# Kernel tuning notes

Hardware: AMD Instinct MI355X
Metric: run time of the kernel (lower is better)

Reference implementation:

```python
import jax, jax.numpy as jnp
import numpy as np

N_LAYERS = 12
N_CH = 256
N_IN = 4
KS = 3
SPECT_CH = 640


def conv1d(x, w, b, dilation):
    # x: [B, T, Cin], w: [K, Cin, Cout] (WIO), SAME padding, given dilation
    y = jax.lax.conv_general_dilated(
        x, w, window_strides=(1,), padding='SAME',
        rhs_dilation=(dilation,), dimension_numbers=('NWC', 'WIO', 'NWC'))
    return y + b


def setup_inputs() -> dict:
    key = jax.random.key(0)
    ks = jax.random.split(key, 16)
    s = 0.02
    inp = {}
    inp['audio'] = jax.random.normal(ks[0], (8, 4096, N_IN), dtype=jnp.float32)
    inp['spect'] = jax.random.normal(ks[1], (8, 4096, SPECT_CH), dtype=jnp.float32)
    # start 1x1 conv: [Cin, Cout]
    inp['w_start'] = jax.random.normal(ks[2], (N_IN, N_CH), dtype=jnp.float32) * s
    inp['b_start'] = jnp.zeros((N_CH,), dtype=jnp.float32)
    # dilated in_layers: stacked [L, K, Cin, 2*Cout]
    inp['w_in'] = jax.random.normal(ks[3], (N_LAYERS, KS, N_CH, 2 * N_CH), dtype=jnp.float32) * s
    inp['b_in'] = jnp.zeros((N_LAYERS, 2 * N_CH), dtype=jnp.float32)
    # cond 1x1 convs: stacked [L, SPECT_CH, 2*Cout]
    inp['w_cond'] = jax.random.normal(ks[4], (N_LAYERS, SPECT_CH, 2 * N_CH), dtype=jnp.float32) * s
    inp['b_cond'] = jnp.zeros((N_LAYERS, 2 * N_CH), dtype=jnp.float32)
    # res_skip 1x1 convs: first L-1 have 2*Cout, last has Cout
    inp['w_res'] = jax.random.normal(ks[5], (N_LAYERS - 1, N_CH, 2 * N_CH), dtype=jnp.float32) * s
    inp['b_res'] = jnp.zeros((N_LAYERS - 1, 2 * N_CH), dtype=jnp.float32)
    inp['w_res_last'] = jax.random.normal(ks[6], (N_CH, N_CH), dtype=jnp.float32) * s
    inp['b_res_last'] = jnp.zeros((N_CH,), dtype=jnp.float32)
    # end 1x1 conv (zero-initialized in the original; use small random for a
    # non-degenerate numerical baseline)
    inp['w_end'] = jax.random.normal(ks[7], (N_CH, 2 * N_IN), dtype=jnp.float32) * s
    inp['b_end'] = jnp.zeros((2 * N_IN,), dtype=jnp.float32)
    return inp


def reference(audio, spect, w_start, b_start, w_in, b_in, w_cond, b_cond,
              w_res, b_res, w_res_last, b_res_last, w_end, b_end):
    # start: 1x1 conv == matmul over channels
    started = jnp.einsum('btc,cd->btd', audio, w_start) + b_start  # [B,T,256]
    # precompute all conditioning projections: [L,B,T,512]
    cond_all = jnp.einsum('btc,lcd->lbtd', spect, w_cond) + b_cond[:, None, None, :]
    output = None
    for i in range(N_LAYERS):
        in_l = conv1d(started, w_in[i], b_in[i], 2 ** i)  # [B,T,512]
        acts = in_l + cond_all[i]
        half_tanh = jnp.tanh(acts[..., :N_CH])
        half_sig = jax.nn.sigmoid(acts[..., N_CH:])
        activated = half_tanh * half_sig  # [B,T,256]
        if i < N_LAYERS - 1:
            rs = jnp.einsum('btc,cd->btd', activated, w_res[i]) + b_res[i]
            started = started + rs[..., :N_CH]
            skip = rs[..., N_CH:]
        else:
            skip = jnp.einsum('btc,cd->btd', activated, w_res_last) + b_res_last
        output = skip if output is None else output + skip
    out = jnp.einsum('btc,cd->btd', output, w_end) + b_end  # [B,T,2*N_IN]
    return out
```

## Files before the change

kernel.cpp:

```cpp
#include <hip/hip_runtime.h>
#include <cstdint>

#define PAD 2048
#define KG 1408

typedef float f32x4 __attribute__((ext_vector_type(4)));
typedef __bf16 bf16x8 __attribute__((ext_vector_type(8)));
typedef __bf16 bf16x4 __attribute__((ext_vector_type(4)));

__device__ __forceinline__ void g2l16(const void* g, void* l) {
    __builtin_amdgcn_global_load_lds(
        (__attribute__((address_space(1))) void*)(uintptr_t)g,
        (__attribute__((address_space(3))) void*)(uint32_t)(uintptr_t)l,
        16, 0, 0);
}


__global__ void cvt_bf16_kernel(const float4* __restrict__ src, bf16x4* __restrict__ dst, int n4) {
    int idx = blockIdx.x * 256 + threadIdx.x;
    if (idx < n4) {
        float4 v = src[idx];
        bf16x4 o = {(__bf16)v.x, (__bf16)v.y, (__bf16)v.z, (__bf16)v.w};
        dst[idx] = o;
    }
}

__global__ void init_started_kernel(const float* __restrict__ audio, const float* __restrict__ w_start,
                                    const float* __restrict__ b_start, __bf16* __restrict__ started_pad) {
    int pr = blockIdx.x * 4 + (threadIdx.x >> 6);
    int c0 = (threadIdx.x & 63) * 4;
    int off = pr & 8191;
    bf16x4 o = {(__bf16)0.f, (__bf16)0.f, (__bf16)0.f, (__bf16)0.f};
    if (off >= PAD && off < PAD + 4096) {
        int r = ((pr >> 13) << 12) + (off - PAD);
        float a0 = audio[r * 4 + 0], a1 = audio[r * 4 + 1], a2 = audio[r * 4 + 2], a3 = audio[r * 4 + 3];
        for (int j = 0; j < 4; ++j) {
            int c = c0 + j;
            o[j] = (__bf16)(b_start[c] + a0 * w_start[c] + a1 * w_start[256 + c]
                            + a2 * w_start[512 + c] + a3 * w_start[768 + c]);
        }
    }
    *(bf16x4*)&started_pad[(size_t)pr * 256 + c0] = o;
}

__global__ void transpose_gate(const float* __restrict__ w_in, const float* __restrict__ w_cond,
                               __bf16* __restrict__ Wg) {
    __shared__ float tile[64][65];
    int i = blockIdx.z;
    int k0 = blockIdx.y * 64, n0 = blockIdx.x * 64;
    int tid = threadIdx.x, c = tid & 63, rr = tid >> 6;
    for (int it = 0; it < 16; ++it) {
        int kl = it * 4 + rr;
        int k = k0 + kl;
        int np = n0 + c;
        int phys = ((np >> 4) & 1) * 256 + (np >> 5) * 16 + (np & 15);
        float v;
        if (k < 768) v = w_in[((i * 3 + (k >> 8)) * 256 + (k & 255)) * 512 + phys];
        else         v = w_cond[(i * 640 + (k - 768)) * 512 + phys];
        tile[kl][c] = v;
    }
    __syncthreads();
    for (int it = 0; it < 16; ++it) {
        int nl = it * 4 + rr;
        Wg[(size_t)(i * 512 + n0 + nl) * KG + k0 + c] = (__bf16)tile[c][nl];
    }
}

__global__ void transpose_kn(const float* __restrict__ src, __bf16* __restrict__ dst,
                             int K, int N, int srcLS, int dstLS) {
    __shared__ float tile[64][65];
    int i = blockIdx.z;
    int k0 = blockIdx.y * 64, n0 = blockIdx.x * 64;
    int tid = threadIdx.x, c = tid & 63, rr = tid >> 6;
    const float* s = src + (size_t)i * srcLS;
    __bf16* dp = dst + (size_t)i * dstLS;
    for (int it = 0; it < 16; ++it) {
        int kl = it * 4 + rr;
        tile[kl][c] = s[(k0 + kl) * N + n0 + c];
    }
    __syncthreads();
    for (int it = 0; it < 16; ++it) {
        int nl = it * 4 + rr;
        dp[(size_t)(n0 + nl) * K + k0 + c] = (__bf16)tile[c][nl];
    }
}

__global__ void bias_gate_kernel(const float* __restrict__ b_in, const float* __restrict__ b_cond,
                                 float* __restrict__ bias) {
    int idx = blockIdx.x * 256 + threadIdx.x;
    int i = idx >> 9, np = idx & 511;
    int phys = ((np >> 4) & 1) * 256 + (np >> 5) * 16 + (np & 15);
    bias[idx] = b_in[i * 512 + phys] + b_cond[i * 512 + phys];
}

__global__ void wfold_kernel(const float* __restrict__ w_res, const float* __restrict__ w_res_last,
                             const float* __restrict__ w_end, const float* __restrict__ b_res,
                             const float* __restrict__ b_res_last, const float* __restrict__ b_end,
                             float* __restrict__ wfold, float* __restrict__ outconst) {
    if (blockIdx.x == 96) {
        __shared__ float red[256][8];
        int j = threadIdx.x;
        float bsum = b_res_last[j];
        for (int i = 0; i < 11; ++i) bsum += b_res[i * 512 + 256 + j];
        for (int c = 0; c < 8; ++c) red[j][c] = bsum * w_end[j * 8 + c];
        __syncthreads();
        if (j < 8) {
            float s = b_end[j];
            for (int t = 0; t < 256; ++t) s += red[t][j];
            outconst[j] = s;
        }
        return;
    }
    int idx = blockIdx.x * 256 + threadIdx.x;
    int i = idx >> 11, rem = idx & 2047, k = rem >> 3, c = rem & 7;
    float s = 0.f;
    if (i < 11) {
        const float* wr = w_res + (size_t)(i * 256 + k) * 512 + 256;
        for (int j = 0; j < 256; ++j) s += wr[j] * w_end[j * 8 + c];
    } else {
        const float* wr = w_res_last + k * 256;
        for (int j = 0; j < 256; ++j) s += wr[j] * w_end[j * 8 + c];
    }
    wfold[idx] = s;
}


__global__ __launch_bounds__(512, 2) void gate_kernel(
    const __bf16* __restrict__ started_pad, const __bf16* __restrict__ spect,
    const __bf16* __restrict__ Wg,
    const float* __restrict__ bias,
    __bf16* __restrict__ activated, int d) {
    __shared__ __align__(16) __bf16 SMEM[65536];
    const int tid = threadIdx.x;
    const int m0 = blockIdx.x * 256;
    const int n0 = blockIdx.y * 256;
    const int padbase = ((m0 >> 12) << 13) + PAD + (m0 & 4095);
    const int wave = tid >> 6, lane = tid & 63;
    const int wr = wave >> 2, wc = wave & 3;
    const int quad = lane >> 4, l15 = lane & 15;

    const int srow = tid >> 2;
    const int scw = ((tid & 3) * 8) ^ (((tid >> 3) & 3) << 3);

    f32x4 acc[8][4];
    #pragma unroll
    for (int i = 0; i < 8; i++)
        #pragma unroll
        for (int j = 0; j < 4; j++) acc[i][j] = f32x4{0.f, 0.f, 0.f, 0.f};

    auto stageA = [&](int kt, int s) {
        const __bf16* g0;
        int rs;
        if (kt < 24) {
            int tap = kt >> 3;
            int cb = (kt & 7) * 32;
            g0 = started_pad + (padbase + (tap - 1) * d) * 256 + cb + scw;
            rs = 256;
        } else {
            int cb = (kt - 24) * 32;
            g0 = spect + (size_t)m0 * 640 + cb + scw;
            rs = 640;
        }
        __bf16* As = SMEM + s * 8192;
        g2l16(g0 + srow * rs, As + tid * 8);
        g2l16(g0 + (128 + srow) * rs, As + 4096 + tid * 8);
    };
    auto stageB = [&](int kt, int s) {
        const __bf16* g0 = Wg + (size_t)(n0 + srow) * KG + kt * 32 + scw;
        __bf16* Bs = SMEM + 32768 + s * 8192;
        g2l16(g0, Bs + tid * 8);
        g2l16(g0 + 128 * KG, Bs + 4096 + tid * 8);
    };

    stageA(0, 0); stageB(0, 0);
    stageA(1, 1); stageB(1, 1);
    asm volatile("s_waitcnt vmcnt(4)" ::: "memory");
    asm volatile("s_barrier" ::: "memory");

    bf16x8 a_cur[4], b_cur[4], b_nxt[4];
    {
        const __bf16* Asl = SMEM;
        const __bf16* Bsl = SMEM + 32768;
        #pragma unroll
        for (int f = 0; f < 4; ++f) {
            int ar = wr * 128 + f * 16 + l15;
            a_cur[f] = *(const bf16x8*)&Asl[ar * 32 + ((quad * 8) ^ (((ar >> 1) & 3) << 3))];
        }
        #pragma unroll
        for (int nf = 0; nf < 4; ++nf) {
            int br = wc * 64 + nf * 16 + l15;
            b_cur[nf] = *(const bf16x8*)&Bsl[br * 32 + ((quad * 8) ^ (((br >> 1) & 3) << 3))];
        }
    }

    for (int j = 0; j < 44; ++j) {
        const int s = j & 3;
        const int sn = (j + 1) & 3;
        const __bf16* Asl = SMEM + s * 8192;

        if (j + 2 < 44) stageA(j + 2, (j + 2) & 3);
        bf16x8 a_nxt[4];
        #pragma unroll
        for (int f = 0; f < 4; ++f) {
            int ar = wr * 128 + 64 + f * 16 + l15;
            a_nxt[f] = *(const bf16x8*)&Asl[ar * 32 + ((quad * 8) ^ (((ar >> 1) & 3) << 3))];
        }
        if (j + 2 < 44) asm volatile("s_waitcnt vmcnt(2)" ::: "memory");
        else            asm volatile("s_waitcnt vmcnt(0)" ::: "memory");
        __builtin_amdgcn_s_setprio(1);
        #pragma unroll
        for (int f = 0; f < 4; ++f)
            #pragma unroll
            for (int nf = 0; nf < 4; ++nf)
                acc[f][nf] = __builtin_amdgcn_mfma_f32_16x16x32_bf16(a_cur[f], b_cur[nf], acc[f][nf], 0, 0, 0);
        __builtin_amdgcn_s_setprio(0);
        asm volatile("s_barrier" ::: "memory");

        if (j + 2 < 44) stageB(j + 2, (j + 2) & 3);
        if (j + 1 < 44) {
            const __bf16* Anl = SMEM + sn * 8192;
            const __bf16* Bnl = SMEM + 32768 + sn * 8192;
            #pragma unroll
            for (int f = 0; f < 4; ++f) {
                int ar = wr * 128 + f * 16 + l15;
                a_cur[f] = *(const bf16x8*)&Anl[ar * 32 + ((quad * 8) ^ (((ar >> 1) & 3) << 3))];
            }
            #pragma unroll
            for (int nf = 0; nf < 4; ++nf) {
                int br = wc * 64 + nf * 16 + l15;
                b_nxt[nf] = *(const bf16x8*)&Bnl[br * 32 + ((quad * 8) ^ (((br >> 1) & 3) << 3))];
            }
        }
        __builtin_amdgcn_s_setprio(1);
        #pragma unroll
        for (int f = 0; f < 4; ++f)
            #pragma unroll
            for (int nf = 0; nf < 4; ++nf)
                acc[4 + f][nf] = __builtin_amdgcn_mfma_f32_16x16x32_bf16(a_nxt[f], b_cur[nf], acc[4 + f][nf], 0, 0, 0);
        __builtin_amdgcn_s_setprio(0);
        if (j + 1 < 44) {
            #pragma unroll
            for (int nf = 0; nf < 4; ++nf) b_cur[nf] = b_nxt[nf];
        }
    }

    __syncthreads();

    __bf16* tile = SMEM;
    #pragma unroll
    for (int nj = 0; nj < 2; ++nj) {
        int colT = wc * 64 + nj * 32 + l15;
        float bt = bias[n0 + colT];
        float bs = bias[n0 + colT + 16];
        int chl = wc * 32 + nj * 16 + l15;
        #pragma unroll
        for (int mi = 0; mi < 8; ++mi) {
            #pragma unroll
            for (int reg = 0; reg < 4; ++reg) {
                int row = wr * 128 + mi * 16 + quad * 4 + reg;
                float xt = acc[mi][2 * nj][reg] + bt;
                float xs = acc[mi][2 * nj + 1][reg] + bs;
                float th = 2.f / (1.f + __expf(-2.f * xt)) - 1.f;
                float sg = 1.f / (1.f + __expf(-xs));
                tile[row * 132 + chl] = (__bf16)(th * sg);
            }
        }
    }
    __syncthreads();
    int chb = n0 >> 1;
    for (int pass = 0; pass < 8; ++pass) {
        int row = (tid >> 4) + 32 * pass;
        int seg = tid & 15;
        bf16x8 v = *(const bf16x8*)&tile[row * 132 + seg * 8];
        *(bf16x8*)&activated[(m0 + row) * 256 + chb + seg * 8] = v;
    }
}

__global__ __launch_bounds__(256) void res_kernel(
    const __bf16* __restrict__ activated, const __bf16* __restrict__ Wr,
    const float* __restrict__ b_res,
    const float* __restrict__ wfold,
    const float* __restrict__ outconst,
    __bf16* __restrict__ started_pad, float* __restrict__ out, int initOut) {
    __shared__ __align__(16) __bf16 As[2][128 * 32];
    __shared__ __align__(16) __bf16 Bs[2][128 * 32];
    __shared__ __align__(16) __bf16 WfB[16 * 264];
    __shared__ __align__(16) float Tile[64 * 132];
    const int tid = threadIdx.x;
    const int m0 = blockIdx.x * 128;
    const int n0 = blockIdx.y * 128;
    const int padbase = ((m0 >> 12) << 13) + PAD + (m0 & 4095);
    const int srow = tid >> 2;
    const int swcol = ((tid & 3) ^ ((srow >> 1) & 3)) * 8;
    const int wave = tid >> 6, lane = tid & 63;
    const int wm = (wave >> 1) * 64, wn = (wave & 1) * 64;
    const int quad = lane >> 4, l15 = lane & 15;
    const bool doOut = (blockIdx.y == 0);
    const bool outWave = doOut && (wn == 0);

    f32x4 acc[4][4];
    for (int i = 0; i < 4; i++)
        for (int j = 0; j < 4; j++) acc[i][j] = f32x4{0.f, 0.f, 0.f, 0.f};
    f32x4 acc_o[4];
    for (int i = 0; i < 4; i++) acc_o[i] = f32x4{0.f, 0.f, 0.f, 0.f};

    const __bf16* Abase = activated + (m0 + srow) * 256 + swcol;
    const __bf16* Bbase = Wr + (n0 + srow) * 256 + swcol;

    auto stage = [&](int ks, int s) {
        int kk = ks * 32;
        g2l16(Abase + kk, &As[s][tid * 8]);
        g2l16(Abase + kk + 64 * 256, &As[s][tid * 8 + 2048]);
        g2l16(Bbase + kk, &Bs[s][tid * 8]);
        g2l16(Bbase + kk + 64 * 256, &Bs[s][tid * 8 + 2048]);
    };

    if (doOut) {
        for (int t = 0; t < 16; ++t) {
            int e = t * 256 + tid;
            int col = e >> 8, k = e & 255;
            WfB[col * 264 + k] = (col < 8) ? (__bf16)wfold[k * 8 + col] : (__bf16)0.f;
        }
    }

    stage(0, 0);
    __syncthreads();

    for (int ks = 0; ks < 8; ++ks) {
        const int cur = ks & 1;
        if (ks + 1 < 8) stage(ks + 1, cur ^ 1);
        bf16x8 a[4], b[4];
        for (int mi = 0; mi < 4; mi++) {
            int row = wm + mi * 16 + l15;
            a[mi] = *(const bf16x8*)&As[cur][row * 32 + ((quad ^ ((row >> 1) & 3)) * 8)];
        }
        for (int ni = 0; ni < 4; ni++) {
            int row = wn + ni * 16 + l15;
            b[ni] = *(const bf16x8*)&Bs[cur][row * 32 + ((quad ^ ((row >> 1) & 3)) * 8)];
        }
        for (int mi = 0; mi < 4; mi++)
            for (int ni = 0; ni < 4; ni++)
                acc[mi][ni] = __builtin_amdgcn_mfma_f32_16x16x32_bf16(a[mi], b[ni], acc[mi][ni], 0, 0, 0);
        if (outWave) {
            bf16x8 bx = *(const bf16x8*)&WfB[l15 * 264 + ks * 32 + quad * 8];
            for (int mi = 0; mi < 4; mi++)
                acc_o[mi] = __builtin_amdgcn_mfma_f32_16x16x32_bf16(a[mi], bx, acc_o[mi], 0, 0, 0);
        }
        __syncthreads();
    }

    for (int half = 0; half < 2; ++half) {
        if ((wm >> 6) == half) {
            for (int ni = 0; ni < 4; ++ni) {
                int colL = wn + ni * 16 + l15;
                float bcol = b_res[n0 + colL];
                for (int mi = 0; mi < 4; ++mi)
                    for (int reg = 0; reg < 4; ++reg)
                        Tile[(mi * 16 + quad * 4 + reg) * 132 + colL] = acc[mi][ni][reg] + bcol;
            }
        }
        __syncthreads();
        int row = tid >> 2;
        int cs = (tid & 3) * 32;
        __bf16* sp = started_pad + (size_t)(padbase + half * 64 + row) * 256 + n0 + cs;
        const float* tp = Tile + row * 132 + cs;
        #pragma unroll
        for (int v = 0; v < 4; ++v) {
            bf16x8 curv = *(const bf16x8*)&sp[v * 8];
            bf16x8 o;
            #pragma unroll
            for (int e = 0; e < 8; ++e) o[e] = (__bf16)((float)curv[e] + tp[v * 8 + e]);
            *(bf16x8*)&sp[v * 8] = o;
        }
        __syncthreads();
    }

    if (outWave && l15 < 8) {
        for (int mi = 0; mi < 4; ++mi) {
            for (int reg = 0; reg < 4; ++reg) {
                int r = m0 + wm + mi * 16 + quad * 4 + reg;
                float base = initOut ? outconst[l15] : out[r * 8 + l15];
                out[r * 8 + l15] = base + acc_o[mi][reg];
            }
        }
    }
}

__global__ __launch_bounds__(256) void outacc_kernel(
    const __bf16* __restrict__ activated, const float* __restrict__ wfold,
    float* __restrict__ out) {
    __shared__ __align__(16) float Wf[2048];
    int tid = threadIdx.x;
    ((float4*)Wf)[tid] = ((const float4*)wfold)[tid];
    ((float4*)Wf)[256 + tid] = ((const float4*)wfold)[256 + tid];
    __syncthreads();
    int row2 = tid >> 1, half = tid & 1;
    int r = blockIdx.x * 128 + row2;
    const bf16x8* ap = (const bf16x8*)(activated + r * 256);
    const float4* wf = (const float4*)Wf;
    float ox = 0.f, oy = 0.f, oz = 0.f, ow = 0.f;
    for (int c8 = 0; c8 < 32; ++c8) {
        bf16x8 av = ap[c8];
        for (int e = 0; e < 8; ++e) {
            float a = (float)av[e];
            float4 w = wf[(c8 * 8 + e) * 2 + half];
            ox += a * w.x; oy += a * w.y; oz += a * w.z; ow += a * w.w;
        }
    }
    float4* op = (float4*)&out[r * 8 + half * 4];
    float4 o = *op;
    o.x += ox; o.y += oy; o.z += oz; o.w += ow;
    *op = o;
}


extern "C" void kernel_launch(void* const* d_in, const int* in_sizes, int n_in,
                              void* d_out, int out_size, void* d_ws, size_t ws_size,
                              hipStream_t stream) {
    const float* audio      = (const float*)d_in[0];
    const float* spect      = (const float*)d_in[1];
    const float* w_start    = (const float*)d_in[2];
    const float* b_start    = (const float*)d_in[3];
    const float* w_in       = (const float*)d_in[4];
    const float* b_in       = (const float*)d_in[5];
    const float* w_cond     = (const float*)d_in[6];
    const float* b_cond     = (const float*)d_in[7];
    const float* w_res      = (const float*)d_in[8];
    const float* b_res      = (const float*)d_in[9];
    const float* w_res_last = (const float*)d_in[10];
    const float* b_res_last = (const float*)d_in[11];
    const float* w_end      = (const float*)d_in[12];
    const float* b_end      = (const float*)d_in[13];
    float* out = (float*)d_out;

    char* ws = (char*)d_ws;
    __bf16* started_pad = (__bf16*)ws; ws += 33554432;
    __bf16* activated   = (__bf16*)ws; ws += 16777216;
    __bf16* spect_bf    = (__bf16*)ws; ws += 41943040;
    __bf16* Wg          = (__bf16*)ws; ws += 17301504;
    __bf16* Wr          = (__bf16*)ws; ws += 1441792;
    float*  wfold       = (float*)ws;  ws += 98304;
    float*  biasg       = (float*)ws;  ws += 24576;
    float*  outconst    = (float*)ws;  ws += 256;

    init_started_kernel<<<dim3(16384), 256, 0, stream>>>(audio, w_start, b_start, started_pad);
    cvt_bf16_kernel<<<dim3(20480), 256, 0, stream>>>((const float4*)spect, (bf16x4*)spect_bf, 5242880);
    transpose_gate<<<dim3(8, 22, 12), 256, 0, stream>>>(w_in, w_cond, Wg);
    transpose_kn<<<dim3(4, 4, 11), 256, 0, stream>>>(w_res, Wr, 256, 512, 256 * 512, 256 * 256);
    bias_gate_kernel<<<dim3(24), 256, 0, stream>>>(b_in, b_cond, biasg);
    wfold_kernel<<<dim3(97), 256, 0, stream>>>(w_res, w_res_last, w_end, b_res, b_res_last, b_end,
                                               wfold, outconst);

    for (int i = 0; i < 12; ++i) {
        gate_kernel<<<dim3(128, 2), 512, 0, stream>>>(
            started_pad, spect_bf, Wg + (size_t)i * 512 * KG, biasg + i * 512, activated, 1 << i);
        if (i < 11) {
            res_kernel<<<dim3(256, 2), 256, 0, stream>>>(
                activated, Wr + (size_t)i * 256 * 256, b_res + i * 512,
                wfold + i * 2048, outconst, started_pad, out, i == 0 ? 1 : 0);
        } else {
            outacc_kernel<<<dim3(256), 256, 0, stream>>>(activated, wfold + 11 * 2048, out);
        }
    }
}
```

Baseline: 1.074 ms.

## Load gate weight fragments directly from global into registers, skipping LDS

The gate GEMM kernel no longer stages the weight (B) tiles through shared memory. Each lane now loads its bf16x8 B fragments straight from global memory one k-step ahead, using ping-pong register buffers in a loop unrolled by two, and the vmcnt waits are adjusted to match. This halves shared memory use, which could allow more blocks per CU, and removes LDS writes and reads for B. The cost is uncoalesced 16-byte global loads strided by rows of KG, extra register pressure, and more reliance on L2 caching of the weights.

```diff
diff --git a/kernel.cpp b/kernel.cpp
--- a/kernel.cpp
+++ b/kernel.cpp
@@ -130,7 +130,7 @@
     const __bf16* __restrict__ Wg,
     const float* __restrict__ bias,
     __bf16* __restrict__ activated, int d) {
-    __shared__ __align__(16) __bf16 SMEM[65536];
+    __shared__ __align__(16) __bf16 SMEM[33792];
     const int tid = threadIdx.x;
     const int m0 = blockIdx.x * 256;
     const int n0 = blockIdx.y * 256;
@@ -141,6 +141,8 @@
 
     const int srow = tid >> 2;
     const int scw = ((tid & 3) * 8) ^ (((tid >> 3) & 3) << 3);
+
+    const __bf16* Bg = Wg + (size_t)(n0 + wc * 64 + l15) * KG + quad * 8;
 
     f32x4 acc[8][4];
     #pragma unroll
@@ -165,84 +167,76 @@
         g2l16(g0 + srow * rs, As + tid * 8);
         g2l16(g0 + (128 + srow) * rs, As + 4096 + tid * 8);
     };
-    auto stageB = [&](int kt, int s) {
-        const __bf16* g0 = Wg + (size_t)(n0 + srow) * KG + kt * 32 + scw;
-        __bf16* Bs = SMEM + 32768 + s * 8192;
-        g2l16(g0, Bs + tid * 8);
-        g2l16(g0 + 128 * KG, Bs + 4096 + tid * 8);
-    };
-
-    stageA(0, 0); stageB(0, 0);
-    stageA(1, 1); stageB(1, 1);
-    asm volatile("s_waitcnt vmcnt(4)" ::: "memory");
+
+    bf16x8 a_cur[4], bE[4], bO[4];
+
+    #pragma unroll
+    for (int nf = 0; nf < 4; ++nf) bE[nf] = *(const bf16x8*)(Bg + nf * 16 * KG);
+    stageA(0, 0);
+    stageA(1, 1);
+    asm volatile("s_waitcnt vmcnt(2)" ::: "memory");
     asm volatile("s_barrier" ::: "memory");
-
-    bf16x8 a_cur[4], b_cur[4], b_nxt[4];
     {
         const __bf16* Asl = SMEM;
-        const __bf16* Bsl = SMEM + 32768;
         #pragma unroll
         for (int f = 0; f < 4; ++f) {
             int ar = wr * 128 + f * 16 + l15;
             a_cur[f] = *(const bf16x8*)&Asl[ar * 32 + ((quad * 8) ^ (((ar >> 1) & 3) << 3))];
         }
-        #pragma unroll
-        for (int nf = 0; nf < 4; ++nf) {
-            int br = wc * 64 + nf * 16 + l15;
-            b_cur[nf] = *(const bf16x8*)&Bsl[br * 32 + ((quad * 8) ^ (((br >> 1) & 3) << 3))];
-        }
-    }
-
-    for (int j = 0; j < 44; ++j) {
-        const int s = j & 3;
-        const int sn = (j + 1) & 3;
-        const __bf16* Asl = SMEM + s * 8192;
-
-        if (j + 2 < 44) stageA(j + 2, (j + 2) & 3);
-        bf16x8 a_nxt[4];
-        #pragma unroll
-        for (int f = 0; f < 4; ++f) {
-            int ar = wr * 128 + 64 + f * 16 + l15;
-            a_nxt[f] = *(const bf16x8*)&Asl[ar * 32 + ((quad * 8) ^ (((ar >> 1) & 3) << 3))];
-        }
-        if (j + 2 < 44) asm volatile("s_waitcnt vmcnt(2)" ::: "memory");
-        else            asm volatile("s_waitcnt vmcnt(0)" ::: "memory");
-        __builtin_amdgcn_s_setprio(1);
-        #pragma unroll
-        for (int f = 0; f < 4; ++f)
-            #pragma unroll
-            for (int nf = 0; nf < 4; ++nf)
-                acc[f][nf] = __builtin_amdgcn_mfma_f32_16x16x32_bf16(a_cur[f], b_cur[nf], acc[f][nf], 0, 0, 0);
-        __builtin_amdgcn_s_setprio(0);
-        asm volatile("s_barrier" ::: "memory");
-
-        if (j + 2 < 44) stageB(j + 2, (j + 2) & 3);
-        if (j + 1 < 44) {
-            const __bf16* Anl = SMEM + sn * 8192;
-            const __bf16* Bnl = SMEM + 32768 + sn * 8192;
-            #pragma unroll
-            for (int f = 0; f < 4; ++f) {
-                int ar = wr * 128 + f * 16 + l15;
-                a_cur[f] = *(const bf16x8*)&Anl[ar * 32 + ((quad * 8) ^ (((ar >> 1) & 3) << 3))];
-            }
-            #pragma unroll
-            for (int nf = 0; nf < 4; ++nf) {
-                int br = wc * 64 + nf * 16 + l15;
-                b_nxt[nf] = *(const bf16x8*)&Bnl[br * 32 + ((quad * 8) ^ (((br >> 1) & 3) << 3))];
-            }
-        }
-        __builtin_amdgcn_s_setprio(1);
-        #pragma unroll
-        for (int f = 0; f < 4; ++f)
-            #pragma unroll
-            for (int nf = 0; nf < 4; ++nf)
-                acc[4 + f][nf] = __builtin_amdgcn_mfma_f32_16x16x32_bf16(a_nxt[f], b_cur[nf], acc[4 + f][nf], 0, 0, 0);
-        __builtin_amdgcn_s_setprio(0);
-        if (j + 1 < 44) {
-            #pragma unroll
-            for (int nf = 0; nf < 4; ++nf) b_cur[nf] = b_nxt[nf];
-        }
-    }
+    }
+
+#define GATE_ITER(j, bcur, bnxt)                                                          \
+    {                                                                                     \
+        const int s = (j) & 3;                                                            \
+        const int sn = ((j) + 1) & 3;                                                     \
+        const __bf16* Asl = SMEM + s * 8192;                                              \
+              \
+        if ((j) + 1 < 44) {                                                               \
+            _Pragma("unroll")                                                             \
+            for (int nf = 0; nf < 4; ++nf)                                                \
+                bnxt[nf] = *(const bf16x8*)(Bg + nf * 16 * KG + ((j) + 1) * 32);          \
+        }                                                                                 \
+        if ((j) + 2 < 44) stageA((j) + 2, ((j) + 2) & 3);                                 \
+        bf16x8 a_nxt[4];                                                                  \
+        _Pragma("unroll")                                                                 \
+        for (int f = 0; f < 4; ++f) {                                                     \
+            int ar = wr * 128 + 64 + f * 16 + l15;                                        \
+            a_nxt[f] = *(const bf16x8*)&Asl[ar * 32 + ((quad * 8) ^ (((ar >> 1) & 3) << 3))]; \
+        }                                                                                 \
+        if ((j) + 2 < 44)      asm volatile("s_waitcnt vmcnt(6)" ::: "memory");           \
+        else if ((j) + 1 < 44) asm volatile("s_waitcnt vmcnt(4)" ::: "memory");           \
+        else                   asm volatile("s_waitcnt vmcnt(0)" ::: "memory");           \
+        __builtin_amdgcn_s_setprio(1);                                                    \
+        _Pragma("unroll")                                                                 \
+        for (int f = 0; f < 4; ++f)                                                       \
+            _Pragma("unroll")                                                             \
+            for (int nf = 0; nf < 4; ++nf)                                                \
+                acc[f][nf] = __builtin_amdgcn_mfma_f32_16x16x32_bf16(a_cur[f], bcur[nf], acc[f][nf], 0, 0, 0); \
+        __builtin_amdgcn_s_setprio(0);                                                    \
+        asm volatile("s_barrier" ::: "memory");              \
+                                              \
+        if ((j) + 1 < 44) {                                                               \
+            const __bf16* Anl = SMEM + sn * 8192;                                         \
+            _Pragma("unroll")                                                             \
+            for (int f = 0; f < 4; ++f) {                                                 \
+                int ar = wr * 128 + f * 16 + l15;                                         \
+                a_cur[f] = *(const bf16x8*)&Anl[ar * 32 + ((quad * 8) ^ (((ar >> 1) & 3) << 3))]; \
+            }                                                                             \
+        }                                                                                 \
+        __builtin_amdgcn_s_setprio(1);                                                    \
+        _Pragma("unroll")                                                                 \
+        for (int f = 0; f < 4; ++f)                                                       \
+            _Pragma("unroll")                                                             \
+            for (int nf = 0; nf < 4; ++nf)                                                \
+                acc[4 + f][nf] = __builtin_amdgcn_mfma_f32_16x16x32_bf16(a_nxt[f], bcur[nf], acc[4 + f][nf], 0, 0, 0); \
+        __builtin_amdgcn_s_setprio(0);                                                    \
+    }
+
+    for (int jj = 0; jj < 44; jj += 2) {
+        GATE_ITER(jj, bE, bO);
+        GATE_ITER(jj + 1, bO, bE);
+    }
+#undef GATE_ITER
 
     __syncthreads();
 
```

After: 1.339 ms. +24.6%, slower.
